# Kernel tuning notes

Measured on AMD Instinct MI355X. Metric: run time of the kernel, lower is better.

The kernel has to match this reference:

```python
import jax, jax.numpy as jnp
import numpy as np

N, C, H, W = 64, 64, 8, 8   # batch, channels (img_net_out_dim), feature-map HxW
E = 256                      # ques_rnn_hidden_dim
G = 512                      # rn_g_dim
FD = 512                     # rn_f_dim
GIN = 2 * (C + 2) + E        # g-MLP input dim = 388
NUM_CLASSES = 2


def _lin(key, din, dout):
    # kaiming-uniform-like init for a Linear stored as (in, out)
    bound = float(np.sqrt(6.0 / din))
    w = jax.random.uniform(key, (din, dout), minval=-bound, maxval=bound, dtype=jnp.float32)
    b = jnp.zeros((dout,), dtype=jnp.float32)
    return w, b


def setup_inputs() -> dict:
    key = jax.random.key(0)
    ks = jax.random.split(key, 9)
    img = jax.random.normal(ks[0], (N, C, H, W), dtype=jnp.float32)
    ques = jax.random.normal(ks[1], (N, E), dtype=jnp.float32)
    g_w1, g_b1 = _lin(ks[2], GIN, G)
    g_w2, g_b2 = _lin(ks[3], G, G)
    g_w3, g_b3 = _lin(ks[4], G, G)
    g_w4, g_b4 = _lin(ks[5], G, G)
    f_w1, f_b1 = _lin(ks[6], G, FD)
    f_w2, f_b2 = _lin(ks[7], FD, FD)
    f_w3, f_b3 = _lin(ks[8], FD, NUM_CLASSES)
    return dict(img=img, ques=ques,
                g_w1=g_w1, g_b1=g_b1, g_w2=g_w2, g_b2=g_b2,
                g_w3=g_w3, g_b3=g_b3, g_w4=g_w4, g_b4=g_b4,
                f_w1=f_w1, f_b1=f_b1, f_w2=f_w2, f_b2=f_b2,
                f_w3=f_w3, f_b3=f_b3)


def _img_to_pairs(img, ques):
    # img: (n, c, h, w), ques: (n, e) -> pairs: (n, hw*hw, 2*(c+2)+e)
    n, c, h, w = img.shape
    hw = h * w
    cells = img.reshape(n, c, hw)
    idx = jnp.arange(hw)
    loc = jnp.stack([idx // w, idx % w], axis=0).astype(img.dtype)  # (2, hw)
    cells = jnp.concatenate([cells, jnp.broadcast_to(loc[None], (n, 2, hw))], axis=1)
    feats = cells.transpose(0, 2, 1)  # (n, hw, c+2)
    fdim = feats.shape[-1]
    one = jnp.broadcast_to(feats[:, :, None, :], (n, hw, hw, fdim))   # object i
    two = jnp.broadcast_to(feats[:, None, :, :], (n, hw, hw, fdim))   # object j
    q = jnp.broadcast_to(ques[:, None, None, :], (n, hw, hw, ques.shape[-1]))
    return jnp.concatenate([one, two, q], axis=-1).reshape(n, hw * hw, -1)


def reference(img, ques, g_w1, g_b1, g_w2, g_b2, g_w3, g_b3, g_w4, g_b4,
              f_w1, f_b1, f_w2, f_b2, f_w3, f_b3):
    pairs = _img_to_pairs(img, ques)                      # (N, HW^2, GIN)
    hdd = jax.nn.relu(pairs @ g_w1 + g_b1)                # shared g-MLP over all pairs
    hdd = jax.nn.relu(hdd @ g_w2 + g_b2)
    hdd = jax.nn.relu(hdd @ g_w3 + g_b3)
    hdd = jax.nn.relu(hdd @ g_w4 + g_b4)
    context = hdd.mean(axis=1)                            # (N, G)
    z = jax.nn.relu(context @ f_w1 + f_b1)                # f-MLP (dropout = identity in eval)
    z = jax.nn.relu(z @ f_w2 + f_b2)
    scores = z @ f_w3 + f_b3                              # (N, 2)
    return jax.nn.log_softmax(scores, axis=1)
```

## Files before the change

kernel.cpp:

```cpp
#include <hip/hip_runtime.h>

typedef unsigned short u16;
typedef unsigned int u32;
typedef _Float16 f16;

using half8 = __attribute__((ext_vector_type(8))) _Float16;
using f32x4 = __attribute__((ext_vector_type(4))) float;
using f32x16 = __attribute__((ext_vector_type(16))) float;


__global__ __launch_bounds__(512) void prep_qc(const float* __restrict__ ques,
                                               const float* __restrict__ gw1,
                                               const float* __restrict__ gb1,
                                               float* __restrict__ Qc,
                                               float* __restrict__ Ctx) {
    const int n = blockIdx.x;
    const int t = threadIdx.x;
    __shared__ float q[256];
    if (t < 256) q[t] = ques[(size_t)n * 256 + t];
    __syncthreads();
    float acc = gb1[t];
    for (int e = 0; e < 256; ++e)
        acc += q[e] * gw1[(size_t)(132 + e) * 512 + t];
    Qc[(size_t)n * 512 + t] = acc;
    Ctx[(size_t)n * 512 + t] = 0.f;
}

__global__ __launch_bounds__(512) void prep_p12(const float* __restrict__ img,
                                                const float* __restrict__ gw1,
                                                const float* __restrict__ Qc,
                                                f16* __restrict__ P1c,
                                                f16* __restrict__ P2c) {
    const int blk = blockIdx.x;
    const int n = blk >> 3;
    const int c0 = (blk & 7) * 8;
    const int t = threadIdx.x;
    __shared__ float feats[8][68];
    for (int idx = t; idx < 8 * 66; idx += 512) {
        int rr = idx / 66, cc = idx % 66, cell = c0 + rr;
        float v;
        if (cc < 64)       v = img[((size_t)(n * 64 + cc)) * 64 + cell];
        else if (cc == 64) v = (float)(cell >> 3);
        else               v = (float)(cell & 7);
        feats[rr][cc] = v;
    }
    __syncthreads();
    const int g = t;
    float a1[8], a2[8];
#pragma unroll
    for (int r = 0; r < 8; ++r) { a1[r] = 0.f; a2[r] = 0.f; }
    for (int c = 0; c < 66; ++c) {
        float wa = gw1[(size_t)c * 512 + g];
        float wb = gw1[(size_t)(66 + c) * 512 + g];
#pragma unroll
        for (int r = 0; r < 8; ++r) {
            a1[r] += feats[r][c] * wa;
            a2[r] += feats[r][c] * wb;
        }
    }
    const float qc = Qc[(size_t)n * 512 + g];
    const size_t cb = (size_t)n * 32768 + (g >> 4) * 1024 + ((g >> 3) & 1) * 512 + (g & 7);
#pragma unroll
    for (int r = 0; r < 8; ++r) {
        P1c[cb + (c0 + r) * 8] = (f16)(a1[r] + qc);
        P2c[cb + (c0 + r) * 8] = (f16)a2[r];
    }
}

__global__ void transpose_w(const float* __restrict__ W2, const float* __restrict__ W3,
                            const float* __restrict__ W4, f16* __restrict__ T2,
                            f16* __restrict__ T3, f16* __restrict__ T4) {
    const int L = blockIdx.z;
    const float* W = (L == 0) ? W2 : ((L == 1) ? W3 : W4);
    f16* T = (L == 0) ? T2 : ((L == 1) ? T3 : T4);
    __shared__ float tile[32][33];
    const int bx = blockIdx.x * 32;
    const int by = blockIdx.y * 32;
    const int tx = threadIdx.x, ty = threadIdx.y;
    for (int r = ty; r < 32; r += 8)
        tile[r][tx] = W[(size_t)(by + r) * 512 + bx + tx];
    __syncthreads();
    for (int r = ty; r < 32; r += 8) {
        const int n = bx + r, k = by + tx;
        T[(size_t)(k >> 4) * 8192 + ((k >> 3) & 1) * 4096 + n * 8 + (k & 7)] =
            (f16)tile[tx][r];
    }
}

__global__ __launch_bounds__(512, 4) void fused_g234(
    const f16* __restrict__ P1c, const f16* __restrict__ P2c,
    const f16* __restrict__ T2, const f16* __restrict__ T3,
    const f16* __restrict__ T4, const float* __restrict__ gb2,
    const float* __restrict__ gb3, const float* __restrict__ gb4,
    float* __restrict__ Ctx) {
    const int tid = threadIdx.x;
    const int lane = tid & 63;
    const int lane31 = lane & 31;
    const int khalf = lane >> 5;
    const int wv = tid >> 6;
    const int b = blockIdx.x;
    const int nb = b >> 6;
    const int i0 = b & 63;

    __shared__ alignas(16) f16 H[32 * 1024];

    const f16* P1b = P1c + (size_t)nb * 32768;
    const f16* P2b = P2c + (size_t)nb * 32768;

    f32x16 acc[2][2];
#pragma unroll
    for (int mi = 0; mi < 2; ++mi)
#pragma unroll
        for (int ni = 0; ni < 2; ++ni)
#pragma unroll
            for (int r = 0; r < 16; ++r)
                acc[mi][ni][r] = 0.f;

    const int aoffE = khalf * 512 + (lane31 ^ khalf) * 8;
    const int aoffO = khalf * 512 + (lane31 ^ (2 | khalf)) * 8;
    const int ybase0 = khalf * 512 + lane31 * 8;
    const int ybase1 = khalf * 512 + (32 + lane31) * 8;
    const int xbase  = khalf * 512 + i0 * 8;
    const u32 boff = (u32)(khalf * 4096 + (wv * 64 + lane31) * 8) * 2u;

    auto mfma4 = [&](half8 a0, half8 a1, half8 b0, half8 b1) {
        __builtin_amdgcn_s_setprio(1);
        acc[0][0] = __builtin_amdgcn_mfma_f32_32x32x16_f16(a0, b0, acc[0][0], 0, 0, 0);
        acc[0][1] = __builtin_amdgcn_mfma_f32_32x32x16_f16(a0, b1, acc[0][1], 0, 0, 0);
        acc[1][0] = __builtin_amdgcn_mfma_f32_32x32x16_f16(a1, b0, acc[1][0], 0, 0, 0);
        acc[1][1] = __builtin_amdgcn_mfma_f32_32x32x16_f16(a1, b1, acc[1][1], 0, 0, 0);
        __builtin_amdgcn_s_setprio(0);
    };

    auto run_layer2 = [&](const f16* __restrict__ T) {
        const char* Tb = (const char*)T;
        u32 vo = boff;
        half8 bA0 = *(const half8*)(Tb + vo);
        half8 bA1 = *(const half8*)(Tb + vo + 512);
        half8 bB0, bB1;
#pragma unroll 1
        for (int k2 = 0; k2 < 16; ++k2) {
            const int cb = k2 * 2048;
            vo += 16384;
            bB0 = *(const half8*)(Tb + vo);
            bB1 = *(const half8*)(Tb + vo + 512);
            {
                half8 x  = *(const half8*)(P1b + cb + xbase);
                half8 y0 = *(const half8*)(P2b + cb + ybase0);
                half8 y1 = *(const half8*)(P2b + cb + ybase1);
                half8 a0 = __builtin_elementwise_max(x + y0, (half8)(f16)0.f);
                half8 a1 = __builtin_elementwise_max(x + y1, (half8)(f16)0.f);
                mfma4(a0, a1, bA0, bA1);
            }
            if (k2 < 15) {
                vo += 16384;
                bA0 = *(const half8*)(Tb + vo);
                bA1 = *(const half8*)(Tb + vo + 512);
            }
            {
                half8 x  = *(const half8*)(P1b + cb + 1024 + xbase);
                half8 y0 = *(const half8*)(P2b + cb + 1024 + ybase0);
                half8 y1 = *(const half8*)(P2b + cb + 1024 + ybase1);
                half8 a0 = __builtin_elementwise_max(x + y0, (half8)(f16)0.f);
                half8 a1 = __builtin_elementwise_max(x + y1, (half8)(f16)0.f);
                mfma4(a0, a1, bB0, bB1);
            }
        }
    };

    auto run_layer = [&](const f16* __restrict__ T) {
        const char* Tb = (const char*)T;
        u32 vo = boff;
        half8 bA0 = *(const half8*)(Tb + vo);
        half8 bA1 = *(const half8*)(Tb + vo + 512);
        half8 bB0, bB1;
#pragma unroll 1
        for (int k2 = 0; k2 < 16; ++k2) {
            const int e0 = aoffE + k2 * 2048;
            vo += 16384;
            bB0 = *(const half8*)(Tb + vo);
            bB1 = *(const half8*)(Tb + vo + 512);
            {
                half8 a0 = *(const half8*)&H[e0];
                half8 a1 = *(const half8*)&H[e0 + 256];
                mfma4(a0, a1, bA0, bA1);
            }
            if (k2 < 15) {
                vo += 16384;
                bA0 = *(const half8*)(Tb + vo);
                bA1 = *(const half8*)(Tb + vo + 512);
            }
            {
                const int o0 = aoffO + k2 * 2048 + 1024;
                half8 a0 = *(const half8*)&H[o0];
                half8 a1 = *(const half8*)&H[o0 + 256];
                mfma4(a0, a1, bB0, bB1);
            }
        }
    };

    auto writeback = [&](const float* __restrict__ bias, bool lead_barrier) {
        float bb[2];
#pragma unroll
        for (int ni = 0; ni < 2; ++ni)
            bb[ni] = bias[wv * 64 + ni * 32 + lane31];
        if (lead_barrier) __syncthreads();
#pragma unroll
        for (int ni = 0; ni < 2; ++ni) {
            const int c = wv * 64 + ni * 32 + lane31;
            const int cbase = (c >> 4) * 1024 + ((c >> 3) & 1) * 512;
            const int fw = (((c >> 4) & 1) << 1) | ((c >> 3) & 1);
            const int j = c & 7;
#pragma unroll
            for (int mi = 0; mi < 2; ++mi) {
#pragma unroll
                for (int r = 0; r < 16; ++r) {
                    const int row = mi * 32 + (r & 3) + 4 * khalf + 8 * (r >> 2);
                    float v = fmaxf(acc[mi][ni][r] + bb[ni], 0.f);
                    H[cbase + (row ^ fw) * 8 + j] = (f16)v;
                    acc[mi][ni][r] = 0.f;
                }
            }
        }
        __syncthreads();
    };

    run_layer2(T2);
    writeback(gb2, false);
    run_layer(T3);
    writeback(gb3, true);
    run_layer(T4);

#pragma unroll
    for (int ni = 0; ni < 2; ++ni) {
        const int col = wv * 64 + ni * 32 + lane31;
        float bb = gb4[col];
        float s = 0.f;
#pragma unroll
        for (int mi = 0; mi < 2; ++mi)
#pragma unroll
            for (int r = 0; r < 16; ++r)
                s += fmaxf(acc[mi][ni][r] + bb, 0.f);
        s += __shfl_xor(s, 32, 64);
        if (khalf == 0)
            atomicAdd(&Ctx[(((size_t)nb) << 9) + col], s);
    }
}

__global__ __launch_bounds__(512) void fmlp_all(
    const float* __restrict__ Ctx,
    const float* __restrict__ fw1, const float* __restrict__ fb1,
    const float* __restrict__ fw2, const float* __restrict__ fb2,
    const float* __restrict__ fw3, const float* __restrict__ fb3,
    float* __restrict__ out) {
    const int n = blockIdx.x;
    const int t = threadIdx.x;
    const int lane = t & 63;
    const int wvv = t >> 6;
    __shared__ float a[512];
    __shared__ float z[512];
    __shared__ float r0[8], r1[8];
    a[t] = Ctx[(size_t)n * 512 + t] * (1.0f / 4096.0f);
    __syncthreads();
    float p = fb1[t];
#pragma unroll 8
    for (int i = 0; i < 512; ++i)
        p += a[i] * fw1[(size_t)i * 512 + t];
    z[t] = fmaxf(p, 0.f);
    __syncthreads();
    p = fb2[t];
#pragma unroll 8
    for (int i = 0; i < 512; ++i)
        p += z[i] * fw2[(size_t)i * 512 + t];
    float z2 = fmaxf(p, 0.f);
    float v0 = z2 * fw3[t * 2];
    float v1 = z2 * fw3[t * 2 + 1];
#pragma unroll
    for (int d = 1; d < 64; d <<= 1) {
        v0 += __shfl_xor(v0, d, 64);
        v1 += __shfl_xor(v1, d, 64);
    }
    if (lane == 0) { r0[wvv] = v0; r1[wvv] = v1; }
    __syncthreads();
    if (t == 0) {
        float s0 = fb3[0], s1 = fb3[1];
#pragma unroll
        for (int w = 0; w < 8; ++w) { s0 += r0[w]; s1 += r1[w]; }
        float m = fmaxf(s0, s1);
        float l = logf(expf(s0 - m) + expf(s1 - m)) + m;
        out[n * 2 + 0] = s0 - l;
        out[n * 2 + 1] = s1 - l;
    }
}

extern "C" void kernel_launch(void* const* d_in, const int* in_sizes, int n_in,
                              void* d_out, int out_size, void* d_ws, size_t ws_size,
                              hipStream_t stream) {
    const float* img  = (const float*)d_in[0];
    const float* ques = (const float*)d_in[1];
    const float* gw1  = (const float*)d_in[2];
    const float* gb1  = (const float*)d_in[3];
    const float* gw2  = (const float*)d_in[4];
    const float* gb2  = (const float*)d_in[5];
    const float* gw3  = (const float*)d_in[6];
    const float* gb3  = (const float*)d_in[7];
    const float* gw4  = (const float*)d_in[8];
    const float* gb4  = (const float*)d_in[9];
    const float* fw1  = (const float*)d_in[10];
    const float* fb1  = (const float*)d_in[11];
    const float* fw2  = (const float*)d_in[12];
    const float* fb2  = (const float*)d_in[13];
    const float* fw3  = (const float*)d_in[14];
    const float* fb3  = (const float*)d_in[15];

    char* ws = (char*)d_ws;
    size_t off = 0;
    f16* P1c = (f16*)(ws + off); off += (size_t)4096 * 512 * 2;
    f16* P2c = (f16*)(ws + off); off += (size_t)4096 * 512 * 2;
    float* Qc  = (float*)(ws + off); off += (size_t)64 * 512 * 4;
    float* Ctx = (float*)(ws + off); off += (size_t)64 * 512 * 4;
    f16* T2 = (f16*)(ws + off); off += (size_t)512 * 512 * 2;
    f16* T3 = (f16*)(ws + off); off += (size_t)512 * 512 * 2;
    f16* T4 = (f16*)(ws + off); off += (size_t)512 * 512 * 2;

    prep_qc<<<64, 512, 0, stream>>>(ques, gw1, gb1, Qc, Ctx);
    prep_p12<<<512, 512, 0, stream>>>(img, gw1, Qc, P1c, P2c);
    transpose_w<<<dim3(16, 16, 3), dim3(32, 8), 0, stream>>>(gw2, gw3, gw4, T2, T3, T4);

    fused_g234<<<4096, 512, 0, stream>>>(P1c, P2c, T2, T3, T4, gb2, gb3, gb4, Ctx);

    fmlp_all<<<64, 512, 0, stream>>>(Ctx, fw1, fb1, fw2, fb2, fw3, fb3, (float*)d_out);
}
```

Before: 580.2 us.

## Merge prep kernels into one launch and stage layer-1 activations in LDS

Folds the three preprocessing kernels (question projection, pair projections, weight transpose) into one launch partitioned by block index. Each pair-projection block now recomputes the question projection itself, so the Qc buffer goes away. In the main fused kernel, the layer-1 relu(P1+P2) tile is built once into shared memory up front, so layer 2 reuses the generic LDS-fed run_layer instead of the global-load variant. This removes launch gaps and repeated global P1/P2 reads inside the MFMA loop, at the cost of a prologue, an extra barrier, and redundant question-projection work (8x per sample).

```diff
diff --git a/kernel.cpp b/kernel.cpp
--- a/kernel.cpp
+++ b/kernel.cpp
@@ -9,81 +9,73 @@
 using f32x16 = __attribute__((ext_vector_type(16))) float;
 
 
-__global__ __launch_bounds__(512) void prep_qc(const float* __restrict__ ques,
-                                               const float* __restrict__ gw1,
-                                               const float* __restrict__ gb1,
-                                               float* __restrict__ Qc,
-                                               float* __restrict__ Ctx) {
-    const int n = blockIdx.x;
-    const int t = threadIdx.x;
-    __shared__ float q[256];
-    if (t < 256) q[t] = ques[(size_t)n * 256 + t];
-    __syncthreads();
-    float acc = gb1[t];
-    for (int e = 0; e < 256; ++e)
-        acc += q[e] * gw1[(size_t)(132 + e) * 512 + t];
-    Qc[(size_t)n * 512 + t] = acc;
-    Ctx[(size_t)n * 512 + t] = 0.f;
-}
-
-__global__ __launch_bounds__(512) void prep_p12(const float* __restrict__ img,
-                                                const float* __restrict__ gw1,
-                                                const float* __restrict__ Qc,
-                                                f16* __restrict__ P1c,
-                                                f16* __restrict__ P2c) {
+__global__ __launch_bounds__(512) void prep_all(
+    const float* __restrict__ img, const float* __restrict__ ques,
+    const float* __restrict__ gw1, const float* __restrict__ gb1,
+    const float* __restrict__ gw2, const float* __restrict__ gw3,
+    const float* __restrict__ gw4,
+    f16* __restrict__ P1c, f16* __restrict__ P2c,
+    f16* __restrict__ T2, f16* __restrict__ T3, f16* __restrict__ T4,
+    float* __restrict__ Ctx) {
     const int blk = blockIdx.x;
-    const int n = blk >> 3;
-    const int c0 = (blk & 7) * 8;
     const int t = threadIdx.x;
     __shared__ float feats[8][68];
-    for (int idx = t; idx < 8 * 66; idx += 512) {
-        int rr = idx / 66, cc = idx % 66, cell = c0 + rr;
-        float v;
-        if (cc < 64)       v = img[((size_t)(n * 64 + cc)) * 64 + cell];
-        else if (cc == 64) v = (float)(cell >> 3);
-        else               v = (float)(cell & 7);
-        feats[rr][cc] = v;
-    }
-    __syncthreads();
-    const int g = t;
-    float a1[8], a2[8];
-#pragma unroll
-    for (int r = 0; r < 8; ++r) { a1[r] = 0.f; a2[r] = 0.f; }
-    for (int c = 0; c < 66; ++c) {
-        float wa = gw1[(size_t)c * 512 + g];
-        float wb = gw1[(size_t)(66 + c) * 512 + g];
+    __shared__ float q[256];
+    __shared__ float tile[32][33];
+
+    if (blk < 512) {
+        const int n = blk >> 3;
+        const int c0 = (blk & 7) * 8;
+        if (t < 256) q[t] = ques[(size_t)n * 256 + t];
+        for (int idx = t; idx < 8 * 66; idx += 512) {
+            int rr = idx / 66, cc = idx % 66, cell = c0 + rr;
+            float v;
+            if (cc < 64)       v = img[((size_t)(n * 64 + cc)) * 64 + cell];
+            else if (cc == 64) v = (float)(cell >> 3);
+            else               v = (float)(cell & 7);
+            feats[rr][cc] = v;
+        }
+        __syncthreads();
+        const int g = t;
+        float qc = gb1[g];
+        for (int e = 0; e < 256; ++e)
+            qc += q[e] * gw1[(size_t)(132 + e) * 512 + g];
+        float a1[8], a2[8];
+#pragma unroll
+        for (int r = 0; r < 8; ++r) { a1[r] = 0.f; a2[r] = 0.f; }
+        for (int c = 0; c < 66; ++c) {
+            float wa = gw1[(size_t)c * 512 + g];
+            float wb = gw1[(size_t)(66 + c) * 512 + g];
+#pragma unroll
+            for (int r = 0; r < 8; ++r) {
+                a1[r] += feats[r][c] * wa;
+                a2[r] += feats[r][c] * wb;
+            }
+        }
+        const size_t cb = (size_t)n * 32768 + (g >> 4) * 1024 + ((g >> 3) & 1) * 512 + (g & 7);
 #pragma unroll
         for (int r = 0; r < 8; ++r) {
-            a1[r] += feats[r][c] * wa;
-            a2[r] += feats[r][c] * wb;
-        }
-    }
-    const float qc = Qc[(size_t)n * 512 + g];
-    const size_t cb = (size_t)n * 32768 + (g >> 4) * 1024 + ((g >> 3) & 1) * 512 + (g & 7);
-#pragma unroll
-    for (int r = 0; r < 8; ++r) {
-        P1c[cb + (c0 + r) * 8] = (f16)(a1[r] + qc);
-        P2c[cb + (c0 + r) * 8] = (f16)a2[r];
-    }
-}
-
-__global__ void transpose_w(const float* __restrict__ W2, const float* __restrict__ W3,
-                            const float* __restrict__ W4, f16* __restrict__ T2,
-                            f16* __restrict__ T3, f16* __restrict__ T4) {
-    const int L = blockIdx.z;
-    const float* W = (L == 0) ? W2 : ((L == 1) ? W3 : W4);
-    f16* T = (L == 0) ? T2 : ((L == 1) ? T3 : T4);
-    __shared__ float tile[32][33];
-    const int bx = blockIdx.x * 32;
-    const int by = blockIdx.y * 32;
-    const int tx = threadIdx.x, ty = threadIdx.y;
-    for (int r = ty; r < 32; r += 8)
-        tile[r][tx] = W[(size_t)(by + r) * 512 + bx + tx];
-    __syncthreads();
-    for (int r = ty; r < 32; r += 8) {
-        const int n = bx + r, k = by + tx;
-        T[(size_t)(k >> 4) * 8192 + ((k >> 3) & 1) * 4096 + n * 8 + (k & 7)] =
-            (f16)tile[tx][r];
+            P1c[cb + (c0 + r) * 8] = (f16)(a1[r] + qc);
+            P2c[cb + (c0 + r) * 8] = (f16)a2[r];
+        }
+        if ((blk & 7) == 0) Ctx[(size_t)n * 512 + t] = 0.f;
+    } else {
+        const int tb = blk - 512;
+        const int L = tb >> 8;
+        const int rem = tb & 255;
+        const int bx = (rem & 15) * 32;
+        const int by = (rem >> 4) * 32;
+        const float* W = (L == 0) ? gw2 : ((L == 1) ? gw3 : gw4);
+        f16* T = (L == 0) ? T2 : ((L == 1) ? T3 : T4);
+        const int tx = t & 31, ty = t >> 5;
+        for (int r = ty; r < 32; r += 16)
+            tile[r][tx] = W[(size_t)(by + r) * 512 + bx + tx];
+        __syncthreads();
+        for (int r = ty; r < 32; r += 16) {
+            const int n = bx + r, k = by + tx;
+            T[(size_t)(k >> 4) * 8192 + ((k >> 3) & 1) * 4096 + n * 8 + (k & 7)] =
+                (f16)tile[tx][r];
+        }
     }
 }
 
@@ -107,6 +99,22 @@
     const f16* P1b = P1c + (size_t)nb * 32768;
     const f16* P2b = P2c + (size_t)nb * 32768;
 
+#pragma unroll
+    for (int u = 0; u < 4; ++u) {
+        const int ks = wv * 4 + u;
+        const int cb = ks * 1024 + khalf * 512;
+        const int f = ((ks & 1) << 1) | khalf;
+        half8 x = *(const half8*)(P1b + cb + i0 * 8);
+#pragma unroll
+        for (int rr = 0; rr < 2; ++rr) {
+            half8 y = *(const half8*)(P2b + cb + (rr * 32 + lane31) * 8);
+            half8 s = x + y;
+            s = __builtin_elementwise_max(s, (half8)(f16)0.f);
+            *(half8*)&H[cb + (rr * 32 + (lane31 ^ f)) * 8] = s;
+        }
+    }
+    __syncthreads();
+
     f32x16 acc[2][2];
 #pragma unroll
     for (int mi = 0; mi < 2; ++mi)
@@ -118,9 +126,6 @@
 
     const int aoffE = khalf * 512 + (lane31 ^ khalf) * 8;
     const int aoffO = khalf * 512 + (lane31 ^ (2 | khalf)) * 8;
-    const int ybase0 = khalf * 512 + lane31 * 8;
-    const int ybase1 = khalf * 512 + (32 + lane31) * 8;
-    const int xbase  = khalf * 512 + i0 * 8;
     const u32 boff = (u32)(khalf * 4096 + (wv * 64 + lane31) * 8) * 2u;
 
     auto mfma4 = [&](half8 a0, half8 a1, half8 b0, half8 b1) {
@@ -130,42 +135,6 @@
         acc[1][0] = __builtin_amdgcn_mfma_f32_32x32x16_f16(a1, b0, acc[1][0], 0, 0, 0);
         acc[1][1] = __builtin_amdgcn_mfma_f32_32x32x16_f16(a1, b1, acc[1][1], 0, 0, 0);
         __builtin_amdgcn_s_setprio(0);
-    };
-
-    auto run_layer2 = [&](const f16* __restrict__ T) {
-        const char* Tb = (const char*)T;
-        u32 vo = boff;
-        half8 bA0 = *(const half8*)(Tb + vo);
-        half8 bA1 = *(const half8*)(Tb + vo + 512);
-        half8 bB0, bB1;
-#pragma unroll 1
-        for (int k2 = 0; k2 < 16; ++k2) {
-            const int cb = k2 * 2048;
-            vo += 16384;
-            bB0 = *(const half8*)(Tb + vo);
-            bB1 = *(const half8*)(Tb + vo + 512);
-            {
-                half8 x  = *(const half8*)(P1b + cb + xbase);
-                half8 y0 = *(const half8*)(P2b + cb + ybase0);
-                half8 y1 = *(const half8*)(P2b + cb + ybase1);
-                half8 a0 = __builtin_elementwise_max(x + y0, (half8)(f16)0.f);
-                half8 a1 = __builtin_elementwise_max(x + y1, (half8)(f16)0.f);
-                mfma4(a0, a1, bA0, bA1);
-            }
-            if (k2 < 15) {
-                vo += 16384;
-                bA0 = *(const half8*)(Tb + vo);
-                bA1 = *(const half8*)(Tb + vo + 512);
-            }
-            {
-                half8 x  = *(const half8*)(P1b + cb + 1024 + xbase);
-                half8 y0 = *(const half8*)(P2b + cb + 1024 + ybase0);
-                half8 y1 = *(const half8*)(P2b + cb + 1024 + ybase1);
-                half8 a0 = __builtin_elementwise_max(x + y0, (half8)(f16)0.f);
-                half8 a1 = __builtin_elementwise_max(x + y1, (half8)(f16)0.f);
-                mfma4(a0, a1, bB0, bB1);
-            }
-        }
     };
 
     auto run_layer = [&](const f16* __restrict__ T) {
@@ -199,12 +168,12 @@
         }
     };
 
-    auto writeback = [&](const float* __restrict__ bias, bool lead_barrier) {
+    auto writeback = [&](const float* __restrict__ bias) {
         float bb[2];
 #pragma unroll
         for (int ni = 0; ni < 2; ++ni)
             bb[ni] = bias[wv * 64 + ni * 32 + lane31];
-        if (lead_barrier) __syncthreads();
+        __syncthreads();
 #pragma unroll
         for (int ni = 0; ni < 2; ++ni) {
             const int c = wv * 64 + ni * 32 + lane31;
@@ -225,10 +194,10 @@
         __syncthreads();
     };
 
-    run_layer2(T2);
-    writeback(gb2, false);
+    run_layer(T2);
+    writeback(gb2);
     run_layer(T3);
-    writeback(gb3, true);
+    writeback(gb3);
     run_layer(T4);
 
 #pragma unroll
@@ -317,15 +286,13 @@
     size_t off = 0;
     f16* P1c = (f16*)(ws + off); off += (size_t)4096 * 512 * 2;
     f16* P2c = (f16*)(ws + off); off += (size_t)4096 * 512 * 2;
-    float* Qc  = (float*)(ws + off); off += (size_t)64 * 512 * 4;
     float* Ctx = (float*)(ws + off); off += (size_t)64 * 512 * 4;
     f16* T2 = (f16*)(ws + off); off += (size_t)512 * 512 * 2;
     f16* T3 = (f16*)(ws + off); off += (size_t)512 * 512 * 2;
     f16* T4 = (f16*)(ws + off); off += (size_t)512 * 512 * 2;
 
-    prep_qc<<<64, 512, 0, stream>>>(ques, gw1, gb1, Qc, Ctx);
-    prep_p12<<<512, 512, 0, stream>>>(img, gw1, Qc, P1c, P2c);
-    transpose_w<<<dim3(16, 16, 3), dim3(32, 8), 0, stream>>>(gw2, gw3, gw4, T2, T3, T4);
+    prep_all<<<1280, 512, 0, stream>>>(img, ques, gw1, gb1, gw2, gw3, gw4,
+                                       P1c, P2c, T2, T3, T4, Ctx);
 
     fused_g234<<<4096, 512, 0, stream>>>(P1c, P2c, T2, T3, T4, gb2, gb3, gb4, Ctx);
 
```

Result: faster. 537.6 us (-7.3%).
